# Kernel optimization log

Hardware: AMD Instinct MI355X
Metric: run time of the kernel (lower is better)

Reference implementation:

```python
import jax, jax.numpy as jnp
import numpy as np

EMBED_DIM = 1024
HEAD_NUM = 16
HEAD_DIM = EMBED_DIM // HEAD_NUM
T, B, S = 2048, 4, 2048


def setup_inputs() -> dict:
    key = jax.random.key(0)
    ks = jax.random.split(key, 11)
    s = 0.02
    return {
        "query": jax.random.normal(ks[0], (T, B, EMBED_DIM), jnp.float32),
        "key": jax.random.normal(ks[1], (S, B, EMBED_DIM), jnp.float32),
        "value": jax.random.normal(ks[2], (S, B, EMBED_DIM), jnp.float32),
        "q_proj_weight": jax.random.normal(ks[3], (EMBED_DIM, EMBED_DIM), jnp.float32) * s,
        "k_proj_weight": jax.random.normal(ks[4], (EMBED_DIM, EMBED_DIM), jnp.float32) * s,
        "v_proj_weight": jax.random.normal(ks[5], (EMBED_DIM, EMBED_DIM), jnp.float32) * s,
        "in_proj_bias": jax.random.normal(ks[6], (3 * EMBED_DIM,), jnp.float32) * s,
        "bias_k": jax.random.normal(ks[7], (1, 1, EMBED_DIM), jnp.float32) * s,
        "bias_v": jax.random.normal(ks[8], (1, 1, EMBED_DIM), jnp.float32) * s,
        "out_proj_weight": jax.random.normal(ks[9], (EMBED_DIM, EMBED_DIM), jnp.float32) * s,
        "out_proj_bias": jax.random.normal(ks[10], (EMBED_DIM,), jnp.float32) * s,
    }


def reference(query, key, value, q_proj_weight, k_proj_weight, v_proj_weight,
              in_proj_bias, bias_k, bias_v, out_proj_weight, out_proj_bias):
    t, b, e = query.shape
    h, hd = HEAD_NUM, HEAD_DIM
    scaling = float(hd) ** -0.5
    # input projections (F.linear: x @ W.T + b)
    q = (query @ q_proj_weight.T + in_proj_bias[:e]) * scaling          # [T,B,E]
    k = key @ k_proj_weight.T + in_proj_bias[e:2 * e]                   # [S,B,E]
    v = value @ v_proj_weight.T + in_proj_bias[2 * e:]                  # [S,B,E]
    # append bias_k / bias_v token along the sequence dim
    k = jnp.concatenate([k, jnp.broadcast_to(bias_k, (1, b, e))], axis=0)  # [S+1,B,E]
    v = jnp.concatenate([v, jnp.broadcast_to(bias_v, (1, b, e))], axis=0)  # [S+1,B,E]
    # split heads: [L, B, E] -> [B*H, L, hd]
    q = q.reshape(t, b * h, hd).transpose(1, 0, 2)
    k = k.reshape(-1, b * h, hd).transpose(1, 0, 2)
    v = v.reshape(-1, b * h, hd).transpose(1, 0, 2)
    # full O(T*S) attention, as in the original bmm->softmax->bmm
    weights = jax.nn.softmax(jnp.einsum('nqd,nkd->nqk', q, k), axis=-1)  # [B*H,T,S+1]
    out = jnp.einsum('nqk,nkd->nqd', weights, v)                         # [B*H,T,hd]
    out = out.transpose(1, 0, 2).reshape(t, b, e)
    out = out @ out_proj_weight.T + out_proj_bias
    avg_weights = weights.sum(axis=1) / h                                # [B*H,S+1]
    return out, avg_weights
```

## Files before the change

kernel.cpp:

```cpp
#include <hip/hip_runtime.h>

#define T_DIM 2048
#define B_DIM 4
#define S_DIM 2048
#define E_DIM 1024
#define H_NUM 16
#define HD    64
#define NH    64
#define SP1   2049
#define SPAD  2112
#define NCHUNK 33
#define NTOKE ((size_t)T_DIM * B_DIM * E_DIM)

typedef short bf16x8 __attribute__((ext_vector_type(8)));
typedef short bf16x4 __attribute__((ext_vector_type(4)));
typedef float f32x4  __attribute__((ext_vector_type(4)));
typedef float f32x16 __attribute__((ext_vector_type(16)));
typedef unsigned int u32;

#define QSCALE 0.18033688011112042f

#if __has_builtin(__builtin_amdgcn_exp2f)
__device__ __forceinline__ float exp2_fast(float x) { return __builtin_amdgcn_exp2f(x); }
#else
__device__ __forceinline__ float exp2_fast(float x) { return __expf(x * 0.6931471805599453f); }
#endif

__device__ __forceinline__ unsigned short f2bf(float x) {
    union { float f; unsigned int u; } v; v.f = x;
    unsigned int r = v.u + 0x7FFFu + ((v.u >> 16) & 1u);
    return (unsigned short)(r >> 16);
}

__device__ __forceinline__ u32 cvtpk_bf16(float lo, float hi) {
    u32 r;
    asm("v_cvt_pk_bf16_f32 %0, %1, %2" : "=v"(r) : "v"(lo), "v"(hi));
    return r;
}
__device__ __forceinline__ void plswap(u32& a, u32& b) {
    asm("v_permlane32_swap_b32 %0, %1" : "+v"(a), "+v"(b));
}

__device__ __forceinline__ void load_lds16(const void* g, void* l) {
    __builtin_amdgcn_global_load_lds(
        (const __attribute__((address_space(1))) unsigned int*)g,
        (__attribute__((address_space(3))) unsigned int*)l, 16, 0, 0);
}

__global__ __launch_bounds__(256)
void cvt_all(const float* __restrict__ q, const float* __restrict__ k,
             const float* __restrict__ v, const float* __restrict__ w0,
             const float* __restrict__ w1, const float* __restrict__ w2,
             const float* __restrict__ w3, short* __restrict__ indst,
             short* __restrict__ wdst, short* __restrict__ k_h,
             short* __restrict__ v_h, const float* __restrict__ bias_k,
             const float* __restrict__ bias_v)
{
    const int y = blockIdx.y;
    if (y < 3) {
        const float* src = (y == 0) ? q : (y == 1) ? k : v;
        short* d = indst + (size_t)y * NTOKE;
        const size_t i = (size_t)blockIdx.x * 256 + threadIdx.x;
        const float4* s = reinterpret_cast<const float4*>(src) + i * 2;
        float4 a = s[0], b = s[1];
        uint4 o;
        o.x = cvtpk_bf16(a.x, a.y); o.y = cvtpk_bf16(a.z, a.w);
        o.z = cvtpk_bf16(b.x, b.y); o.w = cvtpk_bf16(b.z, b.w);
        *(reinterpret_cast<uint4*>(d) + i) = o;
    } else {
        const size_t gi = (size_t)blockIdx.x * 256 + threadIdx.x;
        const size_t per = (size_t)E_DIM * E_DIM / 8;
        if (gi < 4 * per) {
            const int wsel = (int)(gi / per);
            const size_t i = gi % per;
            const float* src = (wsel == 0) ? w0 : (wsel == 1) ? w1 : (wsel == 2) ? w2 : w3;
            short* d = wdst + (size_t)wsel * E_DIM * E_DIM;
            const float4* s = reinterpret_cast<const float4*>(src) + i * 2;
            float4 a = s[0], b = s[1];
            uint4 o;
            o.x = cvtpk_bf16(a.x, a.y); o.y = cvtpk_bf16(a.z, a.w);
            o.z = cvtpk_bf16(b.x, b.y); o.w = cvtpk_bf16(b.z, b.w);
            *(reinterpret_cast<uint4*>(d) + i) = o;
        } else {
            const size_t fi = gi - 4 * per;
            if (fi < (size_t)(SPAD - S_DIM) * NH * HD) {
                const int d   = (int)(fi & 63);
                const int row = (int)((fi >> 6) & 63);
                const int n   = (int)(fi >> 12);
                short bk = 0, bv = 0;
                if (row == 0) {
                    bk = (short)f2bf(bias_k[(n & 15) * HD + d]);
                    bv = (short)f2bf(bias_v[(n & 15) * HD + d]);
                }
                const size_t idx = ((size_t)n * SPAD + S_DIM + row) * HD + d;
                k_h[idx] = bk;
                v_h[idx] = bv;
            }
        }
    }
}

__global__ __launch_bounds__(256, 2)
void gemm_qkv(const short* __restrict__ Abase, const short* __restrict__ Wall,
              const float* __restrict__ biasAll, short* __restrict__ outp)
{
    __shared__ short As[2][128][64];
    __shared__ short Bs[2][128][64];
    const int bm = blockIdx.x, bn = blockIdx.y;
    const int z = blockIdx.z;
    const short* Az = Abase + (size_t)z * NTOKE;
    const short* W  = Wall + (size_t)z * E_DIM * E_DIM;
    const float* bias = biasAll + z * E_DIM;

    const int tid = threadIdx.x;
    const int l = tid & 63, w = tid >> 6;
    const int wr = w >> 1, wc = w & 1;
    const int lr = l & 15, lg = l >> 4;
    const int srow = tid >> 3, scol = (tid & 7) * 8;

    auto stage = [&](int b, int k0) {
#pragma unroll
        for (int r = 0; r < 4; ++r) {
            const int row = r * 32 + srow;
            load_lds16(Az + (size_t)(bm * 128 + row) * E_DIM + k0 + scol, &As[b][row][scol]);
            load_lds16(W + (size_t)(bn * 128 + row) * E_DIM + k0 + scol, &Bs[b][row][scol]);
        }
    };

    stage(0, 0);
    __syncthreads();

    f32x4 acc[4][4] = {};
    int buf = 0;

    for (int k0 = 0; k0 < E_DIM; k0 += 64) {
        if (k0 + 64 < E_DIM) stage(buf ^ 1, k0 + 64);

        __builtin_amdgcn_s_setprio(1);
#pragma unroll
        for (int c = 0; c < 2; ++c) {
            bf16x8 af[4], bf[4];
#pragma unroll
            for (int mi = 0; mi < 4; ++mi)
                af[mi] = *reinterpret_cast<const bf16x8*>(&As[buf][wr * 64 + mi * 16 + lr][c * 32 + lg * 8]);
#pragma unroll
            for (int ni = 0; ni < 4; ++ni)
                bf[ni] = *reinterpret_cast<const bf16x8*>(&Bs[buf][wc * 64 + ni * 16 + lr][c * 32 + lg * 8]);
#pragma unroll
            for (int mi = 0; mi < 4; ++mi)
#pragma unroll
                for (int ni = 0; ni < 4; ++ni)
                    acc[mi][ni] = __builtin_amdgcn_mfma_f32_16x16x32_bf16(
                        af[mi], bf[ni], acc[mi][ni], 0, 0, 0);
        }
        __builtin_amdgcn_s_setprio(0);
        __syncthreads();
        buf ^= 1;
    }

#pragma unroll
    for (int mi = 0; mi < 4; ++mi)
#pragma unroll
        for (int ni = 0; ni < 4; ++ni) {
            const int colg = bn * 128 + wc * 64 + ni * 16 + lr;
            const float bv = bias[colg];
#pragma unroll
            for (int r = 0; r < 4; ++r) {
                const int m = bm * 128 + wr * 64 + mi * 16 + lg * 4 + r;
                float v = acc[mi][ni][r] + bv;
                if (z == 0) v *= QSCALE;
                const int seq = m >> 2, b = m & 3;
                const int head = colg >> 6, d = colg & 63;
                const int sd = (z == 0) ? T_DIM : SPAD;
                short* ob = outp;
                if (z == 1) ob += (size_t)NH * T_DIM * HD;
                else if (z == 2) ob += (size_t)NH * T_DIM * HD + (size_t)NH * SPAD * HD;
                ob[((size_t)(b * 16 + head) * sd + seq) * HD + d] = (short)f2bf(v);
            }
        }
}

__global__ __launch_bounds__(512, 4)
void attn_mfma(const short* __restrict__ q_h, const short* __restrict__ k_h,
               const short* __restrict__ v_h, short* __restrict__ o_h,
               float* __restrict__ m_arr, float* __restrict__ l_arr)
{
    __shared__ short KsD[2][64 * 64];
    __shared__ short VtD[2][64 * 64];

    const int id = blockIdx.x;
    const int xcd = id & 7, slot = id >> 3;
    const int n = xcd * 8 + (slot >> 3);
    const int q0 = (slot & 7) * 256;

    const int tid = threadIdx.x, l = tid & 63, w = tid >> 6;
    const int ql = l & 31;
    const int hi = l >> 5;
    const int qrow = q0 + w * 32 + ql;

    const int krow = tid >> 3, kcg = tid & 7;
    const int kswz = (kcg * 16) ^ ((krow & 7) << 4);
    const int sp = tid & 31, dq = tid >> 5;

    const short* kbase = k_h + (size_t)n * SPAD * HD;
    const short* vbase = v_h + (size_t)n * SPAD * HD;

    bf16x8 aq0, aq1, aq2, aq3;
    {
        const short* qp = q_h + ((size_t)n * T_DIM + qrow) * HD + hi * 8;
        aq0 = *(const bf16x8*)(qp);
        aq1 = *(const bf16x8*)(qp + 16);
        aq2 = *(const bf16x8*)(qp + 32);
        aq3 = *(const bf16x8*)(qp + 48);
    }

    bf16x8 pk  = *(const bf16x8*)(kbase + (size_t)krow * HD + kcg * 8);
    bf16x4 pva = *(const bf16x4*)(vbase + (size_t)(2 * sp) * HD + dq * 4);
    bf16x4 pvb = *(const bf16x4*)(vbase + (size_t)(2 * sp + 1) * HD + dq * 4);
    {
        char* KsB = (char*)KsD[0];
        char* VtB = (char*)VtD[0];
        *(bf16x8*)(KsB + krow * 128 + kswz) = pk;
#pragma unroll
        for (int j = 0; j < 4; ++j) {
            u32 pkd = (u32)(unsigned short)pva[j] | ((u32)(unsigned short)pvb[j] << 16);
            const int d = dq * 4 + j;
            *(u32*)(VtB + d * 128 + ((4 * sp) ^ ((d & 7) << 4))) = pkd;
        }
    }
    __syncthreads();

    float m_run = 0.0f;
    float l_run = 0.0f;
    f32x16 accA, accB;
#pragma unroll
    for (int r = 0; r < 16; ++r) { accA[r] = 0.f; accB[r] = 0.f; }

    for (int kc = 0; kc < NCHUNK; ++kc) {
        const char* KsB = (const char*)KsD[kc & 1];
        const char* VtB = (const char*)VtD[kc & 1];
        const bool more = (kc + 1 < NCHUNK);

        if (more) {
            const int s0n = (kc + 1) * 64;
            pk  = *(const bf16x8*)(kbase + (size_t)(s0n + krow) * HD + kcg * 8);
            pva = *(const bf16x4*)(vbase + (size_t)(s0n + 2 * sp) * HD + dq * 4);
            pvb = *(const bf16x4*)(vbase + (size_t)(s0n + 2 * sp + 1) * HD + dq * 4);
        }

        f32x16 sc0, sc1;
        const float nm = -m_run;
#pragma unroll
        for (int r = 0; r < 16; ++r) { sc0[r] = nm; sc1[r] = nm; }
        __builtin_amdgcn_s_setprio(1);
#pragma unroll
        for (int sl = 0; sl < 4; ++sl) {
            const int cb = ((sl * 32) + hi * 16) ^ ((ql & 7) << 4);
            bf16x8 kf0 = *(const bf16x8*)(KsB + ql * 128 + cb);
            bf16x8 kf1 = *(const bf16x8*)(KsB + (32 + ql) * 128 + cb);
            bf16x8 qf = (sl == 0) ? aq0 : (sl == 1) ? aq1 : (sl == 2) ? aq2 : aq3;
            sc0 = __builtin_amdgcn_mfma_f32_32x32x16_bf16(kf0, qf, sc0, 0, 0, 0);
            sc1 = __builtin_amdgcn_mfma_f32_32x32x16_bf16(kf1, qf, sc1, 0, 0, 0);
        }
        __builtin_amdgcn_s_setprio(0);

        const int s0 = kc * 64;
        if (s0 + 64 > SP1) {
#pragma unroll
            for (int r = 0; r < 16; ++r) {
                const int key = (r & 3) + 8 * (r >> 2) + 4 * hi;
                if (s0 + key >= SP1)      sc0[r] = -1e30f;
                if (s0 + 32 + key >= SP1) sc1[r] = -1e30f;
            }
        }

        float mv[16];
#pragma unroll
        for (int r = 0; r < 16; ++r) mv[r] = fmaxf(sc0[r], sc1[r]);
#pragma unroll
        for (int s = 8; s > 0; s >>= 1)
#pragma unroll
            for (int r = 0; r < s; ++r) mv[r] = fmaxf(mv[r], mv[r + s]);
        const float mx = fmaxf(mv[0], __shfl_xor(mv[0], 32));
        if (!__all(mx <= 8.0f)) {
            const float sh = fmaxf(mx, 0.0f);
            const float fac = exp2_fast(-sh);
            l_run *= fac;
#pragma unroll
            for (int r = 0; r < 16; ++r) {
                accA[r] *= fac; accB[r] *= fac;
                sc0[r] -= sh;   sc1[r] -= sh;
            }
            m_run += sh;
        }
        float p0[16], p1[16];
#pragma unroll
        for (int r = 0; r < 16; ++r) p0[r] = exp2_fast(sc0[r]);
#pragma unroll
        for (int r = 0; r < 16; ++r) p1[r] = exp2_fast(sc1[r]);
        float sv[16];
#pragma unroll
        for (int r = 0; r < 16; ++r) sv[r] = p0[r] + p1[r];
#pragma unroll
        for (int s = 8; s > 0; s >>= 1)
#pragma unroll
            for (int r = 0; r < s; ++r) sv[r] += sv[r + s];
        l_run += sv[0] + __shfl_xor(sv[0], 32);

        union PF { u32 u[4]; bf16x8 v; };
        PF pf0, pf1, pf2, pf3;
        {
            u32 a0 = cvtpk_bf16(p0[0], p0[1]),   b0 = cvtpk_bf16(p0[4], p0[5]);   plswap(a0, b0);
            u32 a1 = cvtpk_bf16(p0[2], p0[3]),   b1 = cvtpk_bf16(p0[6], p0[7]);   plswap(a1, b1);
            u32 a2 = cvtpk_bf16(p0[8], p0[9]),   b2 = cvtpk_bf16(p0[12], p0[13]); plswap(a2, b2);
            u32 a3 = cvtpk_bf16(p0[10], p0[11]), b3 = cvtpk_bf16(p0[14], p0[15]); plswap(a3, b3);
            pf0.u[0] = a0; pf0.u[1] = a1; pf0.u[2] = b0; pf0.u[3] = b1;
            pf1.u[0] = a2; pf1.u[1] = a3; pf1.u[2] = b2; pf1.u[3] = b3;
            u32 c0 = cvtpk_bf16(p1[0], p1[1]),   d0_ = cvtpk_bf16(p1[4], p1[5]);   plswap(c0, d0_);
            u32 c1 = cvtpk_bf16(p1[2], p1[3]),   d1_ = cvtpk_bf16(p1[6], p1[7]);   plswap(c1, d1_);
            u32 c2 = cvtpk_bf16(p1[8], p1[9]),   d2_ = cvtpk_bf16(p1[12], p1[13]); plswap(c2, d2_);
            u32 c3 = cvtpk_bf16(p1[10], p1[11]), d3_ = cvtpk_bf16(p1[14], p1[15]); plswap(c3, d3_);
            pf2.u[0] = c0; pf2.u[1] = c1; pf2.u[2] = d0_; pf2.u[3] = d1_;
            pf3.u[0] = c2; pf3.u[1] = c3; pf3.u[2] = d2_; pf3.u[3] = d3_;
        }

        __builtin_amdgcn_s_setprio(1);
#pragma unroll
        for (int ksl = 0; ksl < 4; ++ksl) {
            const int cb = ((ksl * 32) + hi * 16) ^ ((ql & 7) << 4);
            bf16x8 vf0 = *(const bf16x8*)(VtB + ql * 128 + cb);
            bf16x8 vf1 = *(const bf16x8*)(VtB + (32 + ql) * 128 + cb);
            const bf16x8 pv = (ksl == 0) ? pf0.v : (ksl == 1) ? pf1.v : (ksl == 2) ? pf2.v : pf3.v;
            accA = __builtin_amdgcn_mfma_f32_32x32x16_bf16(vf0, pv, accA, 0, 0, 0);
            accB = __builtin_amdgcn_mfma_f32_32x32x16_bf16(vf1, pv, accB, 0, 0, 0);
        }
        __builtin_amdgcn_s_setprio(0);

        if (more) {
            char* KsN = (char*)KsD[(kc & 1) ^ 1];
            char* VtN = (char*)VtD[(kc & 1) ^ 1];
            *(bf16x8*)(KsN + krow * 128 + kswz) = pk;
#pragma unroll
            for (int j = 0; j < 4; ++j) {
                u32 pkd = (u32)(unsigned short)pva[j] | ((u32)(unsigned short)pvb[j] << 16);
                const int d = dq * 4 + j;
                *(u32*)(VtN + d * 128 + ((4 * sp) ^ ((d & 7) << 4))) = pkd;
            }
            __syncthreads();
        }
    }

    const float il = 1.0f / l_run;
    short* orow = o_h + ((size_t)n * T_DIM + qrow) * HD;
#pragma unroll
    for (int rq = 0; rq < 4; ++rq) {
        uint2 st;
        st.x = cvtpk_bf16(accA[rq * 4 + 0] * il, accA[rq * 4 + 1] * il);
        st.y = cvtpk_bf16(accA[rq * 4 + 2] * il, accA[rq * 4 + 3] * il);
        *(uint2*)(orow + rq * 8 + hi * 4) = st;
        uint2 st2;
        st2.x = cvtpk_bf16(accB[rq * 4 + 0] * il, accB[rq * 4 + 1] * il);
        st2.y = cvtpk_bf16(accB[rq * 4 + 2] * il, accB[rq * 4 + 3] * il);
        *(uint2*)(orow + 32 + rq * 8 + hi * 4) = st2;
    }
    if (hi == 0) {
        m_arr[n * T_DIM + qrow] = m_run;
        l_arr[n * T_DIM + qrow] = l_run;
    }
}

__global__ __launch_bounds__(256)
void tail_fused(const short* __restrict__ q_h, const short* __restrict__ k_h,
                const float* __restrict__ m_arr, const float* __restrict__ l_arr,
                const short* __restrict__ o_h, const short* __restrict__ wob,
                const float* __restrict__ out_b, float* __restrict__ out,
                float* __restrict__ avg_out)
{
    __shared__ char smem[32768];
    const int bid = blockIdx.x;
    const int tid = threadIdx.x;

    if (bid < 2112) {
        short (*Qs)[64][72] = (short(*)[64][72])smem;
        float* msh = (float*)(smem + 18432);
        float* lih = msh + 128;

        const int xcd = bid & 7, slot = bid >> 3;
        const int n = xcd * 8 + slot / 33;
        const int s0 = (slot % 33) * 64;

        const int l = tid & 63, w = tid >> 6;
        const int lr = l & 15, lg = l >> 4;
        const int qr = tid >> 3, qcg = tid & 7;

        const short* qbase = q_h + (size_t)n * T_DIM * HD;

        bf16x8 ak[2];
#pragma unroll
        for (int c = 0; c < 2; ++c)
            ak[c] = *reinterpret_cast<const bf16x8*>(
                k_h + ((size_t)n * SPAD + s0 + w * 16 + lr) * HD + c * 32 + lg * 8);

        bf16x8 qa = *(const bf16x8*)(qbase + (size_t)qr * HD + qcg * 8);
        bf16x8 qb = *(const bf16x8*)(qbase + (size_t)(32 + qr) * HD + qcg * 8);
        float mlv = 0.f;
        if (tid < 64) mlv = m_arr[n * T_DIM + tid];
        else if (tid < 128) mlv = l_arr[n * T_DIM + tid - 64];
        *(bf16x8*)&Qs[0][qr][qcg * 8] = qa;
        *(bf16x8*)&Qs[0][32 + qr][qcg * 8] = qb;
        if (tid < 64) msh[tid] = mlv;
        else if (tid < 128) lih[tid - 64] = 1.0f / mlv;
        __syncthreads();

        float csum[4] = {0.f, 0.f, 0.f, 0.f};

        for (int it = 0; it < T_DIM / 64; ++it) {
            const int buf = it & 1;
            const bool more = (it + 1 < T_DIM / 64);
            if (more) {
                const int qo = (it + 1) * 64;
                qa = *(const bf16x8*)(qbase + (size_t)(qo + qr) * HD + qcg * 8);
                qb = *(const bf16x8*)(qbase + (size_t)(qo + 32 + qr) * HD + qcg * 8);
                if (tid < 64) mlv = m_arr[n * T_DIM + qo + tid];
                else if (tid < 128) mlv = l_arr[n * T_DIM + qo + tid - 64];
            }
            __builtin_amdgcn_s_setprio(1);
#pragma unroll
            for (int qt = 0; qt < 4; ++qt) {
                bf16x8 bq0 = *reinterpret_cast<const bf16x8*>(&Qs[buf][qt * 16 + lr][lg * 8]);
                bf16x8 bq1 = *reinterpret_cast<const bf16x8*>(&Qs[buf][qt * 16 + lr][32 + lg * 8]);
                const float mq = msh[buf * 64 + qt * 16 + lr];
                const float lq = lih[buf * 64 + qt * 16 + lr];
                f32x4 z;
#pragma unroll
                for (int r = 0; r < 4; ++r) z[r] = -mq;
                z = __builtin_amdgcn_mfma_f32_16x16x32_bf16(ak[0], bq0, z, 0, 0, 0);
                z = __builtin_amdgcn_mfma_f32_16x16x32_bf16(ak[1], bq1, z, 0, 0, 0);
#pragma unroll
                for (int r = 0; r < 4; ++r)
                    csum[r] += exp2_fast(z[r]) * lq;
            }
            __builtin_amdgcn_s_setprio(0);
            if (more) {
                *(bf16x8*)&Qs[buf ^ 1][qr][qcg * 8] = qa;
                *(bf16x8*)&Qs[buf ^ 1][32 + qr][qcg * 8] = qb;
                if (tid < 64) msh[(buf ^ 1) * 64 + tid] = mlv;
                else if (tid < 128) lih[(buf ^ 1) * 64 + tid - 64] = 1.0f / mlv;
                __syncthreads();
            }
        }

#pragma unroll
        for (int r = 0; r < 4; ++r) {
            float v = csum[r];
            v += __shfl_xor(v, 1, 16);
            v += __shfl_xor(v, 2, 16);
            v += __shfl_xor(v, 4, 16);
            v += __shfl_xor(v, 8, 16);
            if (lr == 0) {
                const int key = s0 + w * 16 + lg * 4 + r;
                if (key < SP1) avg_out[(size_t)n * SP1 + key] = v * 0.0625f;
            }
        }
    } else {
        short (*As)[64] = (short(*)[64])smem;
        short (*Bs)[64] = (short(*)[64])(smem + 16384);

        const int idx = bid - 2112;
        const int bm = idx & 63, bn = idx >> 6;

        const int l = tid & 63, w = tid >> 6;
        const int wr = w >> 1, wc = w & 1;
        const int lr = l & 15, lg = l >> 4;
        const int srow = tid >> 3, scol = (tid & 7) * 8;

        f32x4 acc[4][4] = {};

        for (int k0 = 0; k0 < E_DIM; k0 += 64) {
#pragma unroll
            for (int r = 0; r < 4; ++r) {
                const int row = r * 32 + srow;
                const int m = bm * 128 + row;
                const short* ga = o_h +
                    ((size_t)((m & 3) * 16 + (k0 >> 6)) * T_DIM + (m >> 2)) * HD + scol;
                load_lds16(ga, &As[row][scol]);
                load_lds16(wob + (size_t)(bn * 128 + row) * E_DIM + k0 + scol, &Bs[row][scol]);
            }
            __syncthreads();

            __builtin_amdgcn_s_setprio(1);
#pragma unroll
            for (int c = 0; c < 2; ++c) {
                bf16x8 af[4], bf[4];
#pragma unroll
                for (int mi = 0; mi < 4; ++mi)
                    af[mi] = *reinterpret_cast<const bf16x8*>(&As[wr * 64 + mi * 16 + lr][c * 32 + lg * 8]);
#pragma unroll
                for (int ni = 0; ni < 4; ++ni)
                    bf[ni] = *reinterpret_cast<const bf16x8*>(&Bs[wc * 64 + ni * 16 + lr][c * 32 + lg * 8]);
#pragma unroll
                for (int mi = 0; mi < 4; ++mi)
#pragma unroll
                    for (int ni = 0; ni < 4; ++ni)
                        acc[mi][ni] = __builtin_amdgcn_mfma_f32_16x16x32_bf16(
                            af[mi], bf[ni], acc[mi][ni], 0, 0, 0);
            }
            __builtin_amdgcn_s_setprio(0);
            __syncthreads();
        }

#pragma unroll
        for (int mi = 0; mi < 4; ++mi)
#pragma unroll
            for (int ni = 0; ni < 4; ++ni) {
                const int colg = bn * 128 + wc * 64 + ni * 16 + lr;
                const float bv = out_b[colg];
#pragma unroll
                for (int r = 0; r < 4; ++r) {
                    const int m = bm * 128 + wr * 64 + mi * 16 + lg * 4 + r;
                    out[(size_t)m * E_DIM + colg] = acc[mi][ni][r] + bv;
                }
            }
    }
}

extern "C" void kernel_launch(void* const* d_in, const int* in_sizes, int n_in,
                              void* d_out, int out_size, void* d_ws, size_t ws_size,
                              hipStream_t stream)
{
    const float* query   = (const float*)d_in[0];
    const float* key     = (const float*)d_in[1];
    const float* value   = (const float*)d_in[2];
    const float* wq      = (const float*)d_in[3];
    const float* wk      = (const float*)d_in[4];
    const float* wv      = (const float*)d_in[5];
    const float* in_bias = (const float*)d_in[6];
    const float* bias_k  = (const float*)d_in[7];
    const float* bias_v  = (const float*)d_in[8];
    const float* wo      = (const float*)d_in[9];
    const float* out_b   = (const float*)d_in[10];
    float* out = (float*)d_out;

    short* wqb    = (short*)d_ws;
    short* wob    = wqb + (size_t)3 * E_DIM * E_DIM;
    short* qkv_bf = wqb + (size_t)4 * E_DIM * E_DIM;
    short* q_h = qkv_bf + 3 * NTOKE;
    short* k_h = q_h + (size_t)NH * T_DIM * HD;
    short* v_h = k_h + (size_t)NH * SPAD * HD;
    short* o_h = v_h + (size_t)NH * SPAD * HD;
    float* m_arr = (float*)(o_h + (size_t)NH * T_DIM * HD);
    float* l_arr = m_arr + (size_t)NH * T_DIM;

    const dim3 blk(256);
    hipLaunchKernelGGL(cvt_all, dim3(4096, 4), blk, 0, stream,
                       query, key, value, wq, wk, wv, wo, qkv_bf, wqb,
                       k_h, v_h, bias_k, bias_v);

    hipLaunchKernelGGL(gemm_qkv, dim3(64, 8, 3), blk, 0, stream,
                       qkv_bf, wqb, in_bias, q_h);
    hipLaunchKernelGGL(attn_mfma, dim3(512), dim3(512), 0, stream,
                       q_h, k_h, v_h, o_h, m_arr, l_arr);
    hipLaunchKernelGGL(tail_fused, dim3(2112 + 512), blk, 0, stream,
                       q_h, k_h, m_arr, l_arr, o_h, wob, out_b,
                       out, out + (size_t)T_DIM * B_DIM * E_DIM);
}
```

Before: 315.2 us.

## Split fused tail into colsum and double-buffered output GEMM kernels

The fused tail kernel, which ran the attention-weight column sums and the output projection GEMM as two block ranges of one launch, is split into two separate launches. The output GEMM gains double-buffered LDS staging so the next K tile is loaded while the current one is multiplied, with two blocks per CU allowed. This removes the shared 32 KB LDS budget and mixed-role scheduling, but adds an extra launch and loses concurrent execution of the two tail workloads.

```diff
diff --git a/kernel.cpp b/kernel.cpp
--- a/kernel.cpp
+++ b/kernel.cpp
@@ -180,6 +180,77 @@
         }
 }
 
+__global__ __launch_bounds__(256, 2)
+void gemm_out(const short* __restrict__ o_h, const short* __restrict__ wob,
+              const float* __restrict__ out_b, float* __restrict__ out)
+{
+    __shared__ short As[2][128][64];
+    __shared__ short Bs[2][128][64];
+    const int bm = blockIdx.x, bn = blockIdx.y;
+
+    const int tid = threadIdx.x;
+    const int l = tid & 63, w = tid >> 6;
+    const int wr = w >> 1, wc = w & 1;
+    const int lr = l & 15, lg = l >> 4;
+    const int srow = tid >> 3, scol = (tid & 7) * 8;
+
+    auto stage = [&](int b, int k0) {
+#pragma unroll
+        for (int r = 0; r < 4; ++r) {
+            const int row = r * 32 + srow;
+            const int m = bm * 128 + row;
+            const short* ga = o_h +
+                ((size_t)((m & 3) * 16 + (k0 >> 6)) * T_DIM + (m >> 2)) * HD + scol;
+            load_lds16(ga, &As[b][row][scol]);
+            load_lds16(wob + (size_t)(bn * 128 + row) * E_DIM + k0 + scol, &Bs[b][row][scol]);
+        }
+    };
+
+    stage(0, 0);
+    __syncthreads();
+
+    f32x4 acc[4][4] = {};
+    int buf = 0;
+
+    for (int k0 = 0; k0 < E_DIM; k0 += 64) {
+        if (k0 + 64 < E_DIM) stage(buf ^ 1, k0 + 64);
+
+        __builtin_amdgcn_s_setprio(1);
+#pragma unroll
+        for (int c = 0; c < 2; ++c) {
+            bf16x8 af[4], bf[4];
+#pragma unroll
+            for (int mi = 0; mi < 4; ++mi)
+                af[mi] = *reinterpret_cast<const bf16x8*>(&As[buf][wr * 64 + mi * 16 + lr][c * 32 + lg * 8]);
+#pragma unroll
+            for (int ni = 0; ni < 4; ++ni)
+                bf[ni] = *reinterpret_cast<const bf16x8*>(&Bs[buf][wc * 64 + ni * 16 + lr][c * 32 + lg * 8]);
+#pragma unroll
+            for (int mi = 0; mi < 4; ++mi)
+#pragma unroll
+                for (int ni = 0; ni < 4; ++ni)
+                    acc[mi][ni] = __builtin_amdgcn_mfma_f32_16x16x32_bf16(
+                        af[mi], bf[ni], acc[mi][ni], 0, 0, 0);
+        }
+        __builtin_amdgcn_s_setprio(0);
+        __syncthreads();
+        buf ^= 1;
+    }
+
+#pragma unroll
+    for (int mi = 0; mi < 4; ++mi)
+#pragma unroll
+        for (int ni = 0; ni < 4; ++ni) {
+            const int colg = bn * 128 + wc * 64 + ni * 16 + lr;
+            const float bv = out_b[colg];
+#pragma unroll
+            for (int r = 0; r < 4; ++r) {
+                const int m = bm * 128 + wr * 64 + mi * 16 + lg * 4 + r;
+                out[(size_t)m * E_DIM + colg] = acc[mi][ni][r] + bv;
+            }
+        }
+}
+
 __global__ __launch_bounds__(512, 4)
 void attn_mfma(const short* __restrict__ q_h, const short* __restrict__ k_h,
                const short* __restrict__ v_h, short* __restrict__ o_h,
@@ -370,157 +441,91 @@
 }
 
 __global__ __launch_bounds__(256)
-void tail_fused(const short* __restrict__ q_h, const short* __restrict__ k_h,
-                const float* __restrict__ m_arr, const float* __restrict__ l_arr,
-                const short* __restrict__ o_h, const short* __restrict__ wob,
-                const float* __restrict__ out_b, float* __restrict__ out,
-                float* __restrict__ avg_out)
+void colsum_mfma(const short* __restrict__ q_h, const short* __restrict__ k_h,
+                 const float* __restrict__ m_arr, const float* __restrict__ l_arr,
+                 float* __restrict__ avg_out)
 {
-    __shared__ char smem[32768];
-    const int bid = blockIdx.x;
-    const int tid = threadIdx.x;
-
-    if (bid < 2112) {
-        short (*Qs)[64][72] = (short(*)[64][72])smem;
-        float* msh = (float*)(smem + 18432);
-        float* lih = msh + 128;
-
-        const int xcd = bid & 7, slot = bid >> 3;
-        const int n = xcd * 8 + slot / 33;
-        const int s0 = (slot % 33) * 64;
-
-        const int l = tid & 63, w = tid >> 6;
-        const int lr = l & 15, lg = l >> 4;
-        const int qr = tid >> 3, qcg = tid & 7;
-
-        const short* qbase = q_h + (size_t)n * T_DIM * HD;
-
-        bf16x8 ak[2];
-#pragma unroll
-        for (int c = 0; c < 2; ++c)
-            ak[c] = *reinterpret_cast<const bf16x8*>(
-                k_h + ((size_t)n * SPAD + s0 + w * 16 + lr) * HD + c * 32 + lg * 8);
-
-        bf16x8 qa = *(const bf16x8*)(qbase + (size_t)qr * HD + qcg * 8);
-        bf16x8 qb = *(const bf16x8*)(qbase + (size_t)(32 + qr) * HD + qcg * 8);
-        float mlv = 0.f;
-        if (tid < 64) mlv = m_arr[n * T_DIM + tid];
-        else if (tid < 128) mlv = l_arr[n * T_DIM + tid - 64];
-        *(bf16x8*)&Qs[0][qr][qcg * 8] = qa;
-        *(bf16x8*)&Qs[0][32 + qr][qcg * 8] = qb;
-        if (tid < 64) msh[tid] = mlv;
-        else if (tid < 128) lih[tid - 64] = 1.0f / mlv;
-        __syncthreads();
-
-        float csum[4] = {0.f, 0.f, 0.f, 0.f};
-
-        for (int it = 0; it < T_DIM / 64; ++it) {
-            const int buf = it & 1;
-            const bool more = (it + 1 < T_DIM / 64);
-            if (more) {
-                const int qo = (it + 1) * 64;
-                qa = *(const bf16x8*)(qbase + (size_t)(qo + qr) * HD + qcg * 8);
-                qb = *(const bf16x8*)(qbase + (size_t)(qo + 32 + qr) * HD + qcg * 8);
-                if (tid < 64) mlv = m_arr[n * T_DIM + qo + tid];
-                else if (tid < 128) mlv = l_arr[n * T_DIM + qo + tid - 64];
-            }
-            __builtin_amdgcn_s_setprio(1);
-#pragma unroll
-            for (int qt = 0; qt < 4; ++qt) {
-                bf16x8 bq0 = *reinterpret_cast<const bf16x8*>(&Qs[buf][qt * 16 + lr][lg * 8]);
-                bf16x8 bq1 = *reinterpret_cast<const bf16x8*>(&Qs[buf][qt * 16 + lr][32 + lg * 8]);
-                const float mq = msh[buf * 64 + qt * 16 + lr];
-                const float lq = lih[buf * 64 + qt * 16 + lr];
-                f32x4 z;
-#pragma unroll
-                for (int r = 0; r < 4; ++r) z[r] = -mq;
-                z = __builtin_amdgcn_mfma_f32_16x16x32_bf16(ak[0], bq0, z, 0, 0, 0);
-                z = __builtin_amdgcn_mfma_f32_16x16x32_bf16(ak[1], bq1, z, 0, 0, 0);
-#pragma unroll
-                for (int r = 0; r < 4; ++r)
-                    csum[r] += exp2_fast(z[r]) * lq;
-            }
-            __builtin_amdgcn_s_setprio(0);
-            if (more) {
-                *(bf16x8*)&Qs[buf ^ 1][qr][qcg * 8] = qa;
-                *(bf16x8*)&Qs[buf ^ 1][32 + qr][qcg * 8] = qb;
-                if (tid < 64) msh[(buf ^ 1) * 64 + tid] = mlv;
-                else if (tid < 128) lih[(buf ^ 1) * 64 + tid - 64] = 1.0f / mlv;
-                __syncthreads();
-            }
-        }
-
-#pragma unroll
-        for (int r = 0; r < 4; ++r) {
-            float v = csum[r];
-            v += __shfl_xor(v, 1, 16);
-            v += __shfl_xor(v, 2, 16);
-            v += __shfl_xor(v, 4, 16);
-            v += __shfl_xor(v, 8, 16);
-            if (lr == 0) {
-                const int key = s0 + w * 16 + lg * 4 + r;
-                if (key < SP1) avg_out[(size_t)n * SP1 + key] = v * 0.0625f;
-            }
-        }
-    } else {
-        short (*As)[64] = (short(*)[64])smem;
-        short (*Bs)[64] = (short(*)[64])(smem + 16384);
-
-        const int idx = bid - 2112;
-        const int bm = idx & 63, bn = idx >> 6;
-
-        const int l = tid & 63, w = tid >> 6;
-        const int wr = w >> 1, wc = w & 1;
-        const int lr = l & 15, lg = l >> 4;
-        const int srow = tid >> 3, scol = (tid & 7) * 8;
-
-        f32x4 acc[4][4] = {};
-
-        for (int k0 = 0; k0 < E_DIM; k0 += 64) {
-#pragma unroll
-            for (int r = 0; r < 4; ++r) {
-                const int row = r * 32 + srow;
-                const int m = bm * 128 + row;
-                const short* ga = o_h +
-                    ((size_t)((m & 3) * 16 + (k0 >> 6)) * T_DIM + (m >> 2)) * HD + scol;
-                load_lds16(ga, &As[row][scol]);
-                load_lds16(wob + (size_t)(bn * 128 + row) * E_DIM + k0 + scol, &Bs[row][scol]);
-            }
+    __shared__ short Qs[2][64][72];
+    __shared__ float msh[2][64];
+    __shared__ float lih[2][64];
+
+    const int id = blockIdx.x;
+    const int xcd = id & 7, slot = id >> 3;
+    const int n = xcd * 8 + slot / 33;
+    const int s0 = (slot % 33) * 64;
+
+    const int tid = threadIdx.x, l = tid & 63, w = tid >> 6;
+    const int lr = l & 15, lg = l >> 4;
+    const int qr = tid >> 3, qcg = tid & 7;
+
+    const short* qbase = q_h + (size_t)n * T_DIM * HD;
+
+    bf16x8 ak[2];
+#pragma unroll
+    for (int c = 0; c < 2; ++c)
+        ak[c] = *reinterpret_cast<const bf16x8*>(
+            k_h + ((size_t)n * SPAD + s0 + w * 16 + lr) * HD + c * 32 + lg * 8);
+
+    bf16x8 qa = *(const bf16x8*)(qbase + (size_t)qr * HD + qcg * 8);
+    bf16x8 qb = *(const bf16x8*)(qbase + (size_t)(32 + qr) * HD + qcg * 8);
+    float mlv = 0.f;
+    if (tid < 64) mlv = m_arr[n * T_DIM + tid];
+    else if (tid < 128) mlv = l_arr[n * T_DIM + tid - 64];
+    *(bf16x8*)&Qs[0][qr][qcg * 8] = qa;
+    *(bf16x8*)&Qs[0][32 + qr][qcg * 8] = qb;
+    if (tid < 64) msh[0][tid] = mlv;
+    else if (tid < 128) lih[0][tid - 64] = 1.0f / mlv;
+    __syncthreads();
+
+    float csum[4] = {0.f, 0.f, 0.f, 0.f};
+
+    for (int it = 0; it < T_DIM / 64; ++it) {
+        const int buf = it & 1;
+        const bool more = (it + 1 < T_DIM / 64);
+        if (more) {
+            const int qo = (it + 1) * 64;
+            qa = *(const bf16x8*)(qbase + (size_t)(qo + qr) * HD + qcg * 8);
+            qb = *(const bf16x8*)(qbase + (size_t)(qo + 32 + qr) * HD + qcg * 8);
+            if (tid < 64) mlv = m_arr[n * T_DIM + qo + tid];
+            else if (tid < 128) mlv = l_arr[n * T_DIM + qo + tid - 64];
+        }
+        __builtin_amdgcn_s_setprio(1);
+#pragma unroll
+        for (int qt = 0; qt < 4; ++qt) {
+            bf16x8 bq0 = *reinterpret_cast<const bf16x8*>(&Qs[buf][qt * 16 + lr][lg * 8]);
+            bf16x8 bq1 = *reinterpret_cast<const bf16x8*>(&Qs[buf][qt * 16 + lr][32 + lg * 8]);
+            const float mq = msh[buf][qt * 16 + lr];
+            const float lq = lih[buf][qt * 16 + lr];
+            f32x4 z;
+#pragma unroll
+            for (int r = 0; r < 4; ++r) z[r] = -mq;
+            z = __builtin_amdgcn_mfma_f32_16x16x32_bf16(ak[0], bq0, z, 0, 0, 0);
+            z = __builtin_amdgcn_mfma_f32_16x16x32_bf16(ak[1], bq1, z, 0, 0, 0);
+#pragma unroll
+            for (int r = 0; r < 4; ++r)
+                csum[r] += exp2_fast(z[r]) * lq;
+        }
+        __builtin_amdgcn_s_setprio(0);
+        if (more) {
+            *(bf16x8*)&Qs[buf ^ 1][qr][qcg * 8] = qa;
+            *(bf16x8*)&Qs[buf ^ 1][32 + qr][qcg * 8] = qb;
+            if (tid < 64) msh[buf ^ 1][tid] = mlv;
+            else if (tid < 128) lih[buf ^ 1][tid - 64] = 1.0f / mlv;
             __syncthreads();
-
-            __builtin_amdgcn_s_setprio(1);
-#pragma unroll
-            for (int c = 0; c < 2; ++c) {
-                bf16x8 af[4], bf[4];
-#pragma unroll
-                for (int mi = 0; mi < 4; ++mi)
-                    af[mi] = *reinterpret_cast<const bf16x8*>(&As[wr * 64 + mi * 16 + lr][c * 32 + lg * 8]);
-#pragma unroll
-                for (int ni = 0; ni < 4; ++ni)
-                    bf[ni] = *reinterpret_cast<const bf16x8*>(&Bs[wc * 64 + ni * 16 + lr][c * 32 + lg * 8]);
-#pragma unroll
-                for (int mi = 0; mi < 4; ++mi)
-#pragma unroll
-                    for (int ni = 0; ni < 4; ++ni)
-                        acc[mi][ni] = __builtin_amdgcn_mfma_f32_16x16x32_bf16(
-                            af[mi], bf[ni], acc[mi][ni], 0, 0, 0);
-            }
-            __builtin_amdgcn_s_setprio(0);
-            __syncthreads();
-        }
-
-#pragma unroll
-        for (int mi = 0; mi < 4; ++mi)
-#pragma unroll
-            for (int ni = 0; ni < 4; ++ni) {
-                const int colg = bn * 128 + wc * 64 + ni * 16 + lr;
-                const float bv = out_b[colg];
-#pragma unroll
-                for (int r = 0; r < 4; ++r) {
-                    const int m = bm * 128 + wr * 64 + mi * 16 + lg * 4 + r;
-                    out[(size_t)m * E_DIM + colg] = acc[mi][ni][r] + bv;
-                }
-            }
+        }
+    }
+
+#pragma unroll
+    for (int r = 0; r < 4; ++r) {
+        float v = csum[r];
+        v += __shfl_xor(v, 1, 16);
+        v += __shfl_xor(v, 2, 16);
+        v += __shfl_xor(v, 4, 16);
+        v += __shfl_xor(v, 8, 16);
+        if (lr == 0) {
+            const int key = s0 + w * 16 + lg * 4 + r;
+            if (key < SP1) avg_out[(size_t)n * SP1 + key] = v * 0.0625f;
+        }
     }
 }
 
@@ -560,7 +565,8 @@
                        qkv_bf, wqb, in_bias, q_h);
     hipLaunchKernelGGL(attn_mfma, dim3(512), dim3(512), 0, stream,
                        q_h, k_h, v_h, o_h, m_arr, l_arr);
-    hipLaunchKernelGGL(tail_fused, dim3(2112 + 512), blk, 0, stream,
-                       q_h, k_h, m_arr, l_arr, o_h, wob, out_b,
-                       out, out + (size_t)T_DIM * B_DIM * E_DIM);
-}
+    hipLaunchKernelGGL(colsum_mfma, dim3(2112), blk, 0, stream,
+                       q_h, k_h, m_arr, l_arr, out + (size_t)T_DIM * B_DIM * E_DIM);
+    hipLaunchKernelGGL(gemm_out, dim3(64, 8), blk, 0, stream,
+                       o_h, wob, out_b, out);
+}
```

After: 289.9 us. -8.0%, faster.
